# Performance work log

Measured on AMD Instinct MI355X. Metric: run time of the kernel, lower is better.

Reference implementation:

```python
import jax, jax.numpy as jnp
import numpy as np

B, C, S = 16384, 32, 12
EPS = 1e-7


def _p622_rotations() -> np.ndarray:
    """The 12 proper rotations of space group P 61 2 2 (point group 622)."""
    mats = []
    # 6-fold rotations about z
    for k in range(6):
        a = k * np.pi / 3.0
        c, s = np.cos(a), np.sin(a)
        mats.append(np.array([[c, -s, 0.0], [s, c, 0.0], [0.0, 0.0, 1.0]]))
    # 6 two-fold axes in the xy-plane at 30-degree increments: R = 2uu^T - I
    for k in range(6):
        a = k * np.pi / 6.0
        u = np.array([np.cos(a), np.sin(a), 0.0])
        mats.append(2.0 * np.outer(u, u) - np.eye(3))
    return np.stack(mats, axis=0).astype(np.float32)  # (12, 3, 3)


def _random_rotations(key, batch_shape):
    """Uniform-ish random SO(3) matrices via QR of Gaussian 3x3 blocks."""
    A = jax.random.normal(key, batch_shape + (3, 3), dtype=jnp.float32)
    Q, R = jnp.linalg.qr(A)
    # make decomposition unique (positive diag of R)
    d = jnp.sign(jnp.diagonal(R, axis1=-2, axis2=-1))
    Q = Q * d[..., None, :]
    # force det = +1 (odd dim: multiplying by -1 flips det sign)
    det = jnp.linalg.det(Q)
    Q = Q * det[..., None, None]
    return Q


def setup_inputs() -> dict:
    key = jax.random.key(0)
    k1, k2 = jax.random.split(key)
    R_pred = _random_rotations(k1, (B, C))   # (B, C, 3, 3)
    R_gt = _random_rotations(k2, (B,))       # (B, 3, 3)
    rot_mats = jnp.asarray(_p622_rotations())  # (S, 3, 3)
    return {"R_pred": R_pred, "R_gt": R_gt, "rot_mats": rot_mats}


def reference(R_pred, R_gt, rot_mats):
    # Compose every symmetry rotation with the ground truth: (B, S, 3, 3)
    R_gt_sym = jnp.einsum('sij,bjk->bsik', rot_mats, R_gt)
    # trace(R_pred @ R_gt_sym^T) = elementwise dot of the two matrices: (B, C, S)
    tr = jnp.einsum('bcij,bsij->bcs', R_pred, R_gt_sym)
    cos = jnp.clip((tr - 1.0) * 0.5, -1.0 + EPS, 1.0 - EPS)
    theta = jnp.arccos(cos)                  # geodesic angle, (B, C, S)
    # min over symmetries, then min over candidates, mean over batch
    best = jnp.min(jnp.min(theta, axis=2), axis=1)  # (B,)
    return jnp.mean(best)
```

## Files before the change

kernel.cpp:

```cpp
#include <hip/hip_runtime.h>
#include <hip/hip_bf16.h>


#define BPB 8
#define BLOCK 256
#define NB 16384
#define NC 32
#define NS 12
#define NBLK (NB / BPB)

__global__ __launch_bounds__(BLOCK) void sym_loss_main(
    const float* __restrict__ R_pred,
    const float* __restrict__ R_gt,
    const float* __restrict__ rot,
    float* __restrict__ partial)
{
    __shared__ float s_rot[NS * 9];
    __shared__ float s_gt[BPB * 9];
    __shared__ float s_pred[BPB * NC * 9];
    __shared__ float s_theta[BPB];

    const int tid = threadIdx.x;
    const int b0 = blockIdx.x * BPB;

    if (tid < NS * 9) s_rot[tid] = rot[tid];
    if (tid < BPB * 9) s_gt[tid] = R_gt[(size_t)b0 * 9 + tid];

    const float4* src = (const float4*)(R_pred + (size_t)b0 * NC * 9);
    float4* dst = (float4*)s_pred;
    #pragma unroll
    for (int i = tid; i < (BPB * NC * 9) / 4; i += BLOCK) dst[i] = src[i];
    __syncthreads();

    const int lb = tid >> 5;
    const float* P = &s_pred[tid * 9];
    const float* G = &s_gt[lb * 9];

    float M[9];
    #pragma unroll
    for (int i = 0; i < 3; ++i)
        #pragma unroll
        for (int j = 0; j < 3; ++j)
            M[i * 3 + j] = fmaf(P[i * 3 + 0], G[j * 3 + 0],
                           fmaf(P[i * 3 + 1], G[j * 3 + 1],
                                P[i * 3 + 2] * G[j * 3 + 2]));

    float mx = -1e30f;
    #pragma unroll
    for (int s = 0; s < NS; ++s) {
        const float* R = &s_rot[s * 9];
        float tr = 0.0f;
        #pragma unroll
        for (int e = 0; e < 9; ++e) tr = fmaf(M[e], R[e], tr);
        mx = fmaxf(mx, tr);
    }

    #pragma unroll
    for (int m = 1; m < 32; m <<= 1) mx = fmaxf(mx, __shfl_xor(mx, m, 64));

    if ((tid & 31) == 0) {
        const float lo = (float)(-1.0 + 1e-7);
        const float hi = (float)( 1.0 - 1e-7);
        float cosv = fminf(fmaxf((mx - 1.0f) * 0.5f, lo), hi);
        s_theta[lb] = acosf(cosv);
    }
    __syncthreads();

    if (tid == 0) {
        float acc = 0.0f;
        #pragma unroll
        for (int i = 0; i < BPB; ++i) acc += s_theta[i];
        partial[blockIdx.x] = acc;
    }
}

__global__ __launch_bounds__(256) void sym_loss_reduce(
    const float* __restrict__ partial,
    float* __restrict__ out)
{
    __shared__ float s_wave[4];
    const int tid = threadIdx.x;

    float acc = 0.0f;
    #pragma unroll
    for (int i = 0; i < NBLK / 256; ++i) acc += partial[tid + i * 256];

    #pragma unroll
    for (int m = 1; m < 64; m <<= 1) acc += __shfl_xor(acc, m, 64);

    if ((tid & 63) == 0) s_wave[tid >> 6] = acc;
    __syncthreads();

    if (tid == 0) {
        float t = s_wave[0] + s_wave[1] + s_wave[2] + s_wave[3];
        *out = t * (1.0f / (float)NB);
    }
}

extern "C" void kernel_launch(void* const* d_in, const int* in_sizes, int n_in,
                              void* d_out, int out_size, void* d_ws, size_t ws_size,
                              hipStream_t stream) {
    const float* R_pred = (const float*)d_in[0];
    const float* R_gt   = (const float*)d_in[1];
    const float* rot    = (const float*)d_in[2];
    float* out = (float*)d_out;
    float* partial = (float*)d_ws;

    sym_loss_main<<<dim3(NBLK), dim3(BLOCK), 0, stream>>>(R_pred, R_gt, rot, partial);
    sym_loss_reduce<<<dim3(1), dim3(256), 0, stream>>>(partial, out);
}
```

Before: 72.35 us.

## Fuse main and reduce kernels with cooperative grid sync, double per-block work

Merges the two kernels into a single cooperative launch that uses a grid-wide sync before block 0 performs the final reduction, removing the second kernel launch. Each block now handles 16 batch elements, with each thread processing two candidate rows, which halves the grid to 1024 blocks and doubles shared memory per block. The approach depends on all 1024 blocks being co-resident for the cooperative launch (launch bounds request 4 blocks per SIMD), and the grid barrier adds its own synchronisation cost.

```diff
diff --git a/kernel.cpp b/kernel.cpp
--- a/kernel.cpp
+++ b/kernel.cpp
@@ -1,24 +1,29 @@
 #include <hip/hip_runtime.h>
 #include <hip/hip_bf16.h>
+#include <hip/hip_cooperative_groups.h>
+
+namespace cg = cooperative_groups;
 
 
-#define BPB 8
+#define BPB 16
 #define BLOCK 256
 #define NB 16384
 #define NC 32
 #define NS 12
 #define NBLK (NB / BPB)
 
-__global__ __launch_bounds__(BLOCK) void sym_loss_main(
+__global__ __launch_bounds__(BLOCK, 4) void sym_loss_fused(
     const float* __restrict__ R_pred,
     const float* __restrict__ R_gt,
     const float* __restrict__ rot,
-    float* __restrict__ partial)
+    float* __restrict__ partial,
+    float* __restrict__ out)
 {
     __shared__ float s_rot[NS * 9];
     __shared__ float s_gt[BPB * 9];
     __shared__ float s_pred[BPB * NC * 9];
     __shared__ float s_theta[BPB];
+    __shared__ float s_wave[4];
 
     const int tid = threadIdx.x;
     const int b0 = blockIdx.x * BPB;
@@ -32,37 +37,41 @@
     for (int i = tid; i < (BPB * NC * 9) / 4; i += BLOCK) dst[i] = src[i];
     __syncthreads();
 
-    const int lb = tid >> 5;
-    const float* P = &s_pred[tid * 9];
-    const float* G = &s_gt[lb * 9];
+    #pragma unroll
+    for (int h = 0; h < 2; ++h) {
+        const int p  = tid + h * BLOCK;
+        const int lb = p >> 5;
+        const float* P = &s_pred[p * 9];
+        const float* G = &s_gt[lb * 9];
 
-    float M[9];
-    #pragma unroll
-    for (int i = 0; i < 3; ++i)
+        float M[9];
         #pragma unroll
-        for (int j = 0; j < 3; ++j)
-            M[i * 3 + j] = fmaf(P[i * 3 + 0], G[j * 3 + 0],
-                           fmaf(P[i * 3 + 1], G[j * 3 + 1],
-                                P[i * 3 + 2] * G[j * 3 + 2]));
+        for (int i = 0; i < 3; ++i)
+            #pragma unroll
+            for (int j = 0; j < 3; ++j)
+                M[i * 3 + j] = fmaf(P[i * 3 + 0], G[j * 3 + 0],
+                               fmaf(P[i * 3 + 1], G[j * 3 + 1],
+                                    P[i * 3 + 2] * G[j * 3 + 2]));
 
-    float mx = -1e30f;
-    #pragma unroll
-    for (int s = 0; s < NS; ++s) {
-        const float* R = &s_rot[s * 9];
-        float tr = 0.0f;
+        float mx = -1e30f;
         #pragma unroll
-        for (int e = 0; e < 9; ++e) tr = fmaf(M[e], R[e], tr);
-        mx = fmaxf(mx, tr);
-    }
+        for (int s = 0; s < NS; ++s) {
+            const float* R = &s_rot[s * 9];
+            float tr = 0.0f;
+            #pragma unroll
+            for (int e = 0; e < 9; ++e) tr = fmaf(M[e], R[e], tr);
+            mx = fmaxf(mx, tr);
+        }
 
-    #pragma unroll
-    for (int m = 1; m < 32; m <<= 1) mx = fmaxf(mx, __shfl_xor(mx, m, 64));
+        #pragma unroll
+        for (int m = 1; m < 32; m <<= 1) mx = fmaxf(mx, __shfl_xor(mx, m, 64));
 
-    if ((tid & 31) == 0) {
-        const float lo = (float)(-1.0 + 1e-7);
-        const float hi = (float)( 1.0 - 1e-7);
-        float cosv = fminf(fmaxf((mx - 1.0f) * 0.5f, lo), hi);
-        s_theta[lb] = acosf(cosv);
+        if ((p & 31) == 0) {
+            const float lo = (float)(-1.0 + 1e-7);
+            const float hi = (float)( 1.0 - 1e-7);
+            float cosv = fminf(fmaxf((mx - 1.0f) * 0.5f, lo), hi);
+            s_theta[lb] = acosf(cosv);
+        }
     }
     __syncthreads();
 
@@ -72,28 +81,22 @@
         for (int i = 0; i < BPB; ++i) acc += s_theta[i];
         partial[blockIdx.x] = acc;
     }
-}
 
-__global__ __launch_bounds__(256) void sym_loss_reduce(
-    const float* __restrict__ partial,
-    float* __restrict__ out)
-{
-    __shared__ float s_wave[4];
-    const int tid = threadIdx.x;
+    cg::this_grid().sync();
 
-    float acc = 0.0f;
-    #pragma unroll
-    for (int i = 0; i < NBLK / 256; ++i) acc += partial[tid + i * 256];
+    if (blockIdx.x == 0) {
+        float acc = 0.0f;
+        #pragma unroll
+        for (int i = 0; i < NBLK / BLOCK; ++i) acc += partial[tid + i * BLOCK];
 
-    #pragma unroll
-    for (int m = 1; m < 64; m <<= 1) acc += __shfl_xor(acc, m, 64);
+        #pragma unroll
+        for (int m = 1; m < 64; m <<= 1) acc += __shfl_xor(acc, m, 64);
 
-    if ((tid & 63) == 0) s_wave[tid >> 6] = acc;
-    __syncthreads();
+        if ((tid & 63) == 0) s_wave[tid >> 6] = acc;
+        __syncthreads();
 
-    if (tid == 0) {
-        float t = s_wave[0] + s_wave[1] + s_wave[2] + s_wave[3];
-        *out = t * (1.0f / (float)NB);
+        if (tid == 0)
+            *out = (s_wave[0] + s_wave[1] + s_wave[2] + s_wave[3]) * (1.0f / (float)NB);
     }
 }
 
@@ -106,6 +109,8 @@
     float* out = (float*)d_out;
     float* partial = (float*)d_ws;
 
-    sym_loss_main<<<dim3(NBLK), dim3(BLOCK), 0, stream>>>(R_pred, R_gt, rot, partial);
-    sym_loss_reduce<<<dim3(1), dim3(256), 0, stream>>>(partial, out);
+    void* args[] = { (void*)&R_pred, (void*)&R_gt, (void*)&rot,
+                     (void*)&partial, (void*)&out };
+    hipLaunchCooperativeKernel((const void*)sym_loss_fused,
+                               dim3(NBLK), dim3(BLOCK), args, 0, stream);
 }
```

Result: slower. 123.8 us (+71.1%).
